# Performance work log

Measured on AMD Instinct MI355X. Metric: run time of the kernel, lower is better.

Reference implementation:

```python
import jax, jax.numpy as jnp
import numpy as np

EPS = 1e-8

def setup_inputs() -> dict:
    key = jax.random.key(0)
    ks = jax.random.split(key, 7)
    B, S, H, NH, V = 4, 2048, 1024, 8, 2048
    sc = 1.0 / np.sqrt(H)
    return {
        "hidden": jax.random.normal(ks[0], (B, S, H), jnp.float32),
        "prior_w": jax.random.normal(ks[1], (H, NH), jnp.float32) * sc,
        "prior_b": jnp.zeros((NH,), jnp.float32),
        "latent_w": jax.random.normal(ks[2], (H, NH * H), jnp.float32) * sc,
        "latent_b": jnp.zeros((NH * H,), jnp.float32),
        "output_w": jax.random.normal(ks[3], (H, V), jnp.float32) * sc,
        "output_b": jnp.zeros((V,), jnp.float32),
    }

def reference(hidden, prior_w, prior_b, latent_w, latent_b, output_w, output_b):
    B, S, H = hidden.shape
    NH = prior_w.shape[1]
    # prior: sigmoid then renormalize over heads
    prior = jax.nn.sigmoid(hidden @ prior_w + prior_b)              # [B,S,NH]
    prior = prior / (prior.sum(-1, keepdims=True) + EPS)
    # latent: linear -> [B,S,NH,H] -> tanh
    latent = jnp.tanh((hidden @ latent_w + latent_b).reshape(B, S, NH, H))
    # per-head softmax over vocab, weighted sum over heads
    logits = jnp.einsum('bsnh,hv->bsnv', latent, output_w) + output_b
    probs = jax.nn.softmax(logits, axis=-1)                          # [B,S,NH,V]
    return jnp.einsum('bsn,bsnv->bsv', prior, probs)
```

## Files before the change

kernel.cpp:

```cpp
#include <hip/hip_runtime.h>
#include <hip/hip_bf16.h>
#include <stdint.h>

typedef _Float16 f16;
typedef _Float16 f16x8 __attribute__((ext_vector_type(8)));
typedef _Float16 f16x4 __attribute__((ext_vector_type(4)));
typedef float f32x4 __attribute__((ext_vector_type(4)));
typedef float f32x16 __attribute__((ext_vector_type(16)));

#define T_TOK 8192
#define H_DIM 1024
#define NHEAD 8
#define V_DIM 2048

__device__ __forceinline__ void gload16(const void* g, void* l) {
  __builtin_amdgcn_global_load_lds(
      (const __attribute__((address_space(1))) void*)(uintptr_t)g,
      (__attribute__((address_space(3))) void*)(unsigned)(uintptr_t)l,
      16, 0, 0);
}

__device__ __forceinline__ float fast_tanh(float x) {
  float xc = fminf(fmaxf(x, -12.f), 12.f);
  float e = __expf(2.f * xc);
  return (e - 1.f) / (e + 1.f);
}

__device__ __forceinline__ void stage_half(const f16* __restrict__ gRowBase,
                                           char* ldsHalf, int tid, int sl8,
                                           int Kd) {
  const int srow = tid >> 3;
  char* wuni = ldsHalf + ((tid >> 6) << 10);
  gload16(gRowBase + (size_t)srow * Kd + sl8, wuni);
  gload16(gRowBase + (size_t)(srow + 64) * Kd + sl8, wuni + 8192);
}

template <int TANH, int NMAJ>
__global__ __launch_bounds__(512, 2) void k_gemm(const f16* __restrict__ A,
                                                 const f16* __restrict__ Bt,
                                                 const float* __restrict__ bias,
                                                 f16* __restrict__ C,
                                                 int M, int N, int K) {
  __shared__ __align__(16) f16 sA[2][16384];
  __shared__ __align__(16) f16 sB[2][16384];
  const int tid = threadIdx.x;
  const int lane = tid & 63;
  const int wid = tid >> 6;
  const int wr = wid >> 2, wc = wid & 3;
  const int gx = gridDim.x, gy = gridDim.y;
  const int id = blockIdx.y * gx + blockIdx.x;
  const int cpx = (gx * gy) >> 3;
  const int sw = (id & 7) * cpx + (id >> 3);
  int m0, n0;
  if (NMAJ) {
    n0 = (sw / gy) * 256;
    m0 = (sw % gy) * 256;
  } else {
    m0 = (sw / gx) * 256;
    n0 = (sw % gx) * 256;
  }
  const int NT = K >> 6;
  const int sl8 = ((tid & 7) ^ ((tid >> 3) & 7)) << 3;
  const int rr31 = lane & 31;
  const int hi = lane >> 5;
  const int l7 = lane & 7;

  const f16* Ag = A + (size_t)m0 * K;
  const f16* Bg = Bt + (size_t)n0 * K;
  char* sAb = (char*)&sA[0][0];
  char* sBb = (char*)&sB[0][0];

  stage_half(Ag, sAb, tid, sl8, K);
  stage_half(Ag + (size_t)128 * K, sAb + 16384, tid, sl8, K);
  stage_half(Bg, sBb, tid, sl8, K);
  stage_half(Bg + (size_t)128 * K, sBb + 16384, tid, sl8, K);
  stage_half(Bg + 64, sBb + 32768, tid, sl8, K);
  stage_half(Bg + (size_t)128 * K + 64, sBb + 32768 + 16384, tid, sl8, K);
  asm volatile("s_waitcnt vmcnt(4)" ::: "memory");
  __builtin_amdgcn_s_barrier();
  __builtin_amdgcn_sched_barrier(0);

  f32x16 acc[4][2] = {};
  f16x8 af0[4], af1[4], bf[2][4];

#define LDA_SET(dst, base, q)                                                  \
  {                                                                            \
    _Pragma("unroll") for (int mi = 0; mi < 4; ++mi) {                         \
      dst[mi] = *(const f16x8*)((base) + wr * 16384 + mi * 4096 + rr31 * 128 + \
                                (((2 * (q) + hi) ^ l7) << 4));                 \
    }                                                                          \
  }
#define LDB(base)                                                              \
  {                                                                            \
    _Pragma("unroll") for (int n = 0; n < 2; ++n) {                            \
      _Pragma("unroll") for (int ks = 0; ks < 4; ++ks) {                       \
        bf[n][ks] = *(const f16x8*)((base) + wc * 8192 + n * 4096 +            \
                                    rr31 * 128 + (((2 * ks + hi) ^ l7) << 4)); \
      }                                                                        \
    }                                                                          \
  }
#define MFMA8(ks, S)                                                           \
  {                                                                            \
    __builtin_amdgcn_s_setprio(1);                                             \
    _Pragma("unroll") for (int mi = 0; mi < 4; ++mi) {                         \
      _Pragma("unroll") for (int n = 0; n < 2; ++n) {                          \
        acc[mi][n] = __builtin_amdgcn_mfma_f32_32x32x16_f16(                   \
            S[mi], bf[n][ks], acc[mi][n], 0, 0, 0);                            \
      }                                                                        \
    }                                                                          \
    __builtin_amdgcn_s_setprio(0);                                             \
  }

  LDA_SET(af0, sAb, 0);

#define HALF(tt, bc)                                                           \
  {                                                                            \
    const char* cA = sAb + (bc)*32768;                                         \
    const char* cB = sBb + (bc)*32768;                                         \
    char* nA = sAb + ((bc) ^ 1) * 32768;                                       \
    char* nB = sBb + (bc)*32768;                                               \
    const int ktA = ((tt) + 1) << 6, ktB = ((tt) + 2) << 6;                    \
    const bool doA = (tt) + 1 < NT, doB = (tt) + 2 < NT;                       \
                                                                      \
    if (doA) stage_half(Ag + ktA, nA, tid, sl8, K);                            \
    LDB(cB);                                                                   \
    LDA_SET(af1, cA, 1);                                                       \
    __builtin_amdgcn_sched_barrier(0);                                         \
    MFMA8(0, af0);                                                             \
    __builtin_amdgcn_s_barrier();                                              \
                                                                      \
    if (doA) stage_half(Ag + (size_t)128 * K + ktA, nA + 16384, tid, sl8, K);  \
    LDA_SET(af0, cA, 2);                                                       \
    __builtin_amdgcn_sched_barrier(0);                                         \
    MFMA8(1, af1);                                                             \
    __builtin_amdgcn_s_barrier();                                              \
                                                                      \
    if (doB) stage_half(Bg + ktB, nB, tid, sl8, K);                            \
    LDA_SET(af1, cA, 3);                                                       \
    __builtin_amdgcn_sched_barrier(0);                                         \
    MFMA8(2, af0);                                                             \
    __builtin_amdgcn_s_barrier();                                              \
                  \
    if (doB) stage_half(Bg + (size_t)128 * K + ktB, nB + 16384, tid, sl8, K);  \
    if (doB) {                                                                 \
      asm volatile("s_waitcnt vmcnt(4)" ::: "memory");                         \
    } else {                                                                   \
      asm volatile("s_waitcnt vmcnt(0)" ::: "memory");                         \
    }                                                                          \
    __builtin_amdgcn_s_barrier();                                              \
    __builtin_amdgcn_sched_barrier(0);                                         \
    if (doA) LDA_SET(af0, sAb + ((bc) ^ 1) * 32768, 0);                        \
    __builtin_amdgcn_sched_barrier(0);                                         \
    MFMA8(3, af1);                                                             \
  }

#pragma unroll 1
  for (int T = 0; T < NT; T += 2) {
    HALF(T, 0);
    HALF(T + 1, 1);
  }
#undef HALF
#undef LDA_SET
#undef LDB
#undef MFMA8

  const int ccol0 = n0 + wc * 64 + rr31;
  float bv[2];
#pragma unroll
  for (int n = 0; n < 2; ++n) bv[n] = bias[ccol0 + n * 32];
#pragma unroll
  for (int mi = 0; mi < 4; ++mi) {
#pragma unroll
    for (int rq = 0; rq < 4; ++rq) {
#pragma unroll
      for (int r2 = 0; r2 < 4; ++r2) {
        const int row = m0 + wr * 128 + mi * 32 + r2 + 8 * rq + 4 * hi;
        f16* Crow = C + (size_t)row * N;
#pragma unroll
        for (int n = 0; n < 2; ++n) {
          float v = acc[mi][n][rq * 4 + r2] + bv[n];
          if (TANH) v = fast_tanh(v);
          Crow[ccol0 + n * 32] = (f16)v;
        }
      }
    }
  }
}

__global__ __launch_bounds__(256) void k_convert(const float* __restrict__ in,
                                                 f16* __restrict__ out, int n4) {
  int i = blockIdx.x * blockDim.x + threadIdx.x;
  if (i >= n4) return;
  const float4 v = ((const float4*)in)[i];
  f16x4 o;
  o[0] = (f16)v.x; o[1] = (f16)v.y; o[2] = (f16)v.z; o[3] = (f16)v.w;
  ((f16x4*)out)[i] = o;
}

__global__ __launch_bounds__(256) void k_transpose(const float* __restrict__ in,
                                                   f16* __restrict__ out,
                                                   int R, int C) {
  __shared__ f16 tile[64][66];
  const int c0 = blockIdx.x * 64, r0 = blockIdx.y * 64;
  const int tid = threadIdx.x;
  const int tr = tid >> 4;
  const int tc4 = (tid & 15) * 4;
#pragma unroll
  for (int i = 0; i < 4; ++i) {
    const int r = tr + i * 16;
    const float4 v = *(const float4*)&in[(size_t)(r0 + r) * C + c0 + tc4];
    tile[tc4 + 0][r] = (f16)v.x;
    tile[tc4 + 1][r] = (f16)v.y;
    tile[tc4 + 2][r] = (f16)v.z;
    tile[tc4 + 3][r] = (f16)v.w;
  }
  __syncthreads();
  const int oc = tid >> 2;
  const int or4 = (tid & 3) * 16;
#pragma unroll
  for (int i = 0; i < 4; ++i) {
    f16x4 w;
    w[0] = tile[oc][or4 + i * 4 + 0];
    w[1] = tile[oc][or4 + i * 4 + 1];
    w[2] = tile[oc][or4 + i * 4 + 2];
    w[3] = tile[oc][or4 + i * 4 + 3];
    *(f16x4*)&out[(size_t)(c0 + oc) * R + r0 + or4 + i * 4] = w;
  }
}

__global__ __launch_bounds__(256) void k_prior(const float* __restrict__ hidden,
                                               const float* __restrict__ pw,
                                               const float* __restrict__ pb,
                                               float* __restrict__ prior) {
  const int wid = threadIdx.x >> 6, lane = threadIdx.x & 63;
  const int t = blockIdx.x * 4 + wid;
  float acc[NHEAD] = {0.f, 0.f, 0.f, 0.f, 0.f, 0.f, 0.f, 0.f};
  const float* hrow = hidden + (size_t)t * H_DIM;
  for (int k = lane; k < H_DIM; k += 64) {
    float x = hrow[k];
    const float* wr = pw + k * NHEAD;
#pragma unroll
    for (int h = 0; h < NHEAD; ++h) acc[h] += x * wr[h];
  }
#pragma unroll
  for (int h = 0; h < NHEAD; ++h) {
#pragma unroll
    for (int off = 32; off >= 1; off >>= 1) acc[h] += __shfl_xor(acc[h], off);
  }
  if (lane == 0) {
    float p[NHEAD], s = 0.f;
#pragma unroll
    for (int h = 0; h < NHEAD; ++h) {
      p[h] = 1.f / (1.f + __expf(-(acc[h] + pb[h])));
      s += p[h];
    }
    float inv = 1.f / (s + 1e-8f);
#pragma unroll
    for (int h = 0; h < NHEAD; ++h) prior[t * NHEAD + h] = p[h] * inv;
  }
}

__global__ __launch_bounds__(256) void k_softmax(const f16* __restrict__ logits,
                                                 const float* __restrict__ prior,
                                                 float* __restrict__ out) {
  __shared__ float redsm[NHEAD * 4];
  const int t = blockIdx.x;
  const int tid = threadIdx.x, lane = tid & 63, wid = tid >> 6;
  const f16* base = logits + (size_t)t * NHEAD * V_DIM + tid * 8;

  f16x8 x[NHEAD];
#pragma unroll
  for (int h = 0; h < NHEAD; ++h) x[h] = *(const f16x8*)(base + h * V_DIM);

  float xv[NHEAD][8];
  float sml[NHEAD];
#pragma unroll
  for (int h = 0; h < NHEAD; ++h) {
    float s = 0.f;
#pragma unroll
    for (int j = 0; j < 8; ++j) {
      xv[h][j] = __expf(fminf((float)x[h][j], 50.f));
      s += xv[h][j];
    }
    sml[h] = s;
  }
#pragma unroll
  for (int h = 0; h < NHEAD; ++h) {
#pragma unroll
    for (int off = 32; off >= 1; off >>= 1) sml[h] += __shfl_xor(sml[h], off);
  }
  if (lane == 0) {
#pragma unroll
    for (int h = 0; h < NHEAD; ++h) redsm[h * 4 + wid] = sml[h];
  }
  __syncthreads();

  float oa[8] = {0.f, 0.f, 0.f, 0.f, 0.f, 0.f, 0.f, 0.f};
#pragma unroll
  for (int h = 0; h < NHEAD; ++h) {
    const float s = redsm[h * 4 + 0] + redsm[h * 4 + 1] + redsm[h * 4 + 2] +
                    redsm[h * 4 + 3];
    const float coef = prior[t * NHEAD + h] / s;
#pragma unroll
    for (int j = 0; j < 8; ++j) oa[j] += coef * xv[h][j];
  }
  float4* op = (float4*)(out + (size_t)t * V_DIM + tid * 8);
  op[0] = make_float4(oa[0], oa[1], oa[2], oa[3]);
  op[1] = make_float4(oa[4], oa[5], oa[6], oa[7]);
}

extern "C" void kernel_launch(void* const* d_in, const int* in_sizes, int n_in,
                              void* d_out, int out_size, void* d_ws, size_t ws_size,
                              hipStream_t stream) {
  const float* hidden   = (const float*)d_in[0];
  const float* prior_w  = (const float*)d_in[1];
  const float* prior_b  = (const float*)d_in[2];
  const float* latent_w = (const float*)d_in[3];
  const float* latent_b = (const float*)d_in[4];
  const float* output_w = (const float*)d_in[5];
  const float* output_b = (const float*)d_in[6];
  float* out = (float*)d_out;

  char* ws = (char*)d_ws;
  size_t off = 0;
  auto alloc = [&](size_t bytes) -> void* {
    void* p = ws + off;
    off += (bytes + 255) & ~(size_t)255;
    return p;
  };
  f16* hidden_h = (f16*)alloc((size_t)T_TOK * H_DIM * 2);
  f16* lw_t     = (f16*)alloc((size_t)NHEAD * H_DIM * H_DIM * 2);
  f16* ow_t     = (f16*)alloc((size_t)V_DIM * H_DIM * 2);
  float* prior  = (float*)alloc((size_t)T_TOK * NHEAD * 4);

  int tc = T_TOK;
  while (tc > 256) {
    size_t need = off + (size_t)tc * NHEAD * H_DIM * 2 + 256 +
                  (size_t)tc * NHEAD * V_DIM * 2 + 256;
    if (need <= ws_size) break;
    tc >>= 1;
  }
  f16* latent_h = (f16*)alloc((size_t)tc * NHEAD * H_DIM * 2);
  f16* logits_h = (f16*)alloc((size_t)tc * NHEAD * V_DIM * 2);

  k_convert<<<(T_TOK * H_DIM / 4 + 255) / 256, 256, 0, stream>>>(
      hidden, hidden_h, T_TOK * H_DIM / 4);
  k_transpose<<<dim3(NHEAD * H_DIM / 64, H_DIM / 64), 256, 0, stream>>>(
      latent_w, lw_t, H_DIM, NHEAD * H_DIM);
  k_transpose<<<dim3(V_DIM / 64, H_DIM / 64), 256, 0, stream>>>(
      output_w, ow_t, H_DIM, V_DIM);
  k_prior<<<T_TOK / 4, 256, 0, stream>>>(hidden, prior_w, prior_b, prior);

  const int nchunk = T_TOK / tc;
  for (int c = 0; c < nchunk; ++c) {
    const f16* Ah = hidden_h + (size_t)c * tc * H_DIM;
    k_gemm<1, 1><<<dim3(NHEAD * H_DIM / 256, tc / 256), 512, 0, stream>>>(
        Ah, lw_t, latent_b, latent_h, tc, NHEAD * H_DIM, H_DIM);
    k_gemm<0, 0><<<dim3(V_DIM / 256, tc * NHEAD / 256), 512, 0, stream>>>(
        latent_h, ow_t, output_b, logits_h, tc * NHEAD, V_DIM, H_DIM);
    k_softmax<<<tc, 256, 0, stream>>>(logits_h, prior + (size_t)c * tc * NHEAD,
                                      out + (size_t)c * tc * V_DIM);
  }
}
```

Before: 572.6 us.

## Fuse prior with hidden conversion, restructure GEMM grid and chunk logits buffer

Merges the fp32-to-fp16 hidden conversion into the prior kernel, so the hidden tensor is read once instead of twice. The latent GEMM now runs as a single launch over all tokens, using a 3D grid with a fixed 8-column swizzle and a z-dimension that selects the N block. The logits GEMM and softmax run over token quarters sized to fit the workspace, with softmax taking a token offset. This removes one kernel launch and changes the chunking plan, but the full latent buffer must fit in the workspace.

```diff
diff --git a/kernel.cpp b/kernel.cpp
--- a/kernel.cpp
+++ b/kernel.cpp
@@ -35,7 +35,7 @@
   gload16(gRowBase + (size_t)(srow + 64) * Kd + sl8, wuni + 8192);
 }
 
-template <int TANH, int NMAJ>
+template <int TANH>
 __global__ __launch_bounds__(512, 2) void k_gemm(const f16* __restrict__ A,
                                                  const f16* __restrict__ Bt,
                                                  const float* __restrict__ bias,
@@ -47,18 +47,11 @@
   const int lane = tid & 63;
   const int wid = tid >> 6;
   const int wr = wid >> 2, wc = wid & 3;
-  const int gx = gridDim.x, gy = gridDim.y;
-  const int id = blockIdx.y * gx + blockIdx.x;
-  const int cpx = (gx * gy) >> 3;
+  const int id = blockIdx.y * 8 + blockIdx.x;
+  const int cpx = gridDim.y;
   const int sw = (id & 7) * cpx + (id >> 3);
-  int m0, n0;
-  if (NMAJ) {
-    n0 = (sw / gy) * 256;
-    m0 = (sw % gy) * 256;
-  } else {
-    m0 = (sw / gx) * 256;
-    n0 = (sw % gx) * 256;
-  }
+  const int m0 = (sw >> 3) * 256;
+  const int n0 = blockIdx.z * 2048 + (sw & 7) * 256;
   const int NT = K >> 6;
   const int sl8 = ((tid & 7) ^ ((tid >> 3) & 7)) << 3;
   const int rr31 = lane & 31;
@@ -187,16 +180,6 @@
   }
 }
 
-__global__ __launch_bounds__(256) void k_convert(const float* __restrict__ in,
-                                                 f16* __restrict__ out, int n4) {
-  int i = blockIdx.x * blockDim.x + threadIdx.x;
-  if (i >= n4) return;
-  const float4 v = ((const float4*)in)[i];
-  f16x4 o;
-  o[0] = (f16)v.x; o[1] = (f16)v.y; o[2] = (f16)v.z; o[3] = (f16)v.w;
-  ((f16x4*)out)[i] = o;
-}
-
 __global__ __launch_bounds__(256) void k_transpose(const float* __restrict__ in,
                                                    f16* __restrict__ out,
                                                    int R, int C) {
@@ -228,19 +211,30 @@
   }
 }
 
-__global__ __launch_bounds__(256) void k_prior(const float* __restrict__ hidden,
-                                               const float* __restrict__ pw,
-                                               const float* __restrict__ pb,
-                                               float* __restrict__ prior) {
+__global__ __launch_bounds__(256) void k_prior_conv(const float* __restrict__ hidden,
+                                                    const float* __restrict__ pw,
+                                                    const float* __restrict__ pb,
+                                                    float* __restrict__ prior,
+                                                    f16* __restrict__ hidden_h) {
   const int wid = threadIdx.x >> 6, lane = threadIdx.x & 63;
   const int t = blockIdx.x * 4 + wid;
+  const float* hrow = hidden + (size_t)t * H_DIM;
+  f16* orow = hidden_h + (size_t)t * H_DIM;
   float acc[NHEAD] = {0.f, 0.f, 0.f, 0.f, 0.f, 0.f, 0.f, 0.f};
-  const float* hrow = hidden + (size_t)t * H_DIM;
-  for (int k = lane; k < H_DIM; k += 64) {
-    float x = hrow[k];
-    const float* wr = pw + k * NHEAD;
-#pragma unroll
-    for (int h = 0; h < NHEAD; ++h) acc[h] += x * wr[h];
+#pragma unroll
+  for (int i = 0; i < 4; ++i) {
+    const int k = i * 256 + lane * 4;
+    const float4 v = *(const float4*)(hrow + k);
+    f16x4 o;
+    o[0] = (f16)v.x; o[1] = (f16)v.y; o[2] = (f16)v.z; o[3] = (f16)v.w;
+    *(f16x4*)(orow + k) = o;
+    const float vv[4] = {v.x, v.y, v.z, v.w};
+#pragma unroll
+    for (int j = 0; j < 4; ++j) {
+      const float* wr = pw + (size_t)(k + j) * NHEAD;
+#pragma unroll
+      for (int h = 0; h < NHEAD; ++h) acc[h] += vv[j] * wr[h];
+    }
   }
 #pragma unroll
   for (int h = 0; h < NHEAD; ++h) {
@@ -262,11 +256,13 @@
 
 __global__ __launch_bounds__(256) void k_softmax(const f16* __restrict__ logits,
                                                  const float* __restrict__ prior,
-                                                 float* __restrict__ out) {
+                                                 float* __restrict__ out,
+                                                 int t0) {
   __shared__ float redsm[NHEAD * 4];
-  const int t = blockIdx.x;
+  const int tl = blockIdx.x;
+  const int t = t0 + tl;
   const int tid = threadIdx.x, lane = tid & 63, wid = tid >> 6;
-  const f16* base = logits + (size_t)t * NHEAD * V_DIM + tid * 8;
+  const f16* base = logits + (size_t)tl * NHEAD * V_DIM + tid * 8;
 
   f16x8 x[NHEAD];
 #pragma unroll
@@ -332,33 +328,28 @@
   f16* lw_t     = (f16*)alloc((size_t)NHEAD * H_DIM * H_DIM * 2);
   f16* ow_t     = (f16*)alloc((size_t)V_DIM * H_DIM * 2);
   float* prior  = (float*)alloc((size_t)T_TOK * NHEAD * 4);
-
-  int tc = T_TOK;
-  while (tc > 256) {
-    size_t need = off + (size_t)tc * NHEAD * H_DIM * 2 + 256 +
-                  (size_t)tc * NHEAD * V_DIM * 2 + 256;
-    if (need <= ws_size) break;
-    tc >>= 1;
-  }
-  f16* latent_h = (f16*)alloc((size_t)tc * NHEAD * H_DIM * 2);
-  f16* logits_h = (f16*)alloc((size_t)tc * NHEAD * V_DIM * 2);
-
-  k_convert<<<(T_TOK * H_DIM / 4 + 255) / 256, 256, 0, stream>>>(
-      hidden, hidden_h, T_TOK * H_DIM / 4);
+  f16* latent_h = (f16*)alloc((size_t)T_TOK * NHEAD * H_DIM * 2);
+
+  int TQ = 2048;
+  while (TQ > 256 && off + (size_t)TQ * NHEAD * V_DIM * 2 > ws_size) TQ >>= 1;
+  f16* logits_q = (f16*)alloc((size_t)TQ * NHEAD * V_DIM * 2);
+
+  k_prior_conv<<<T_TOK / 4, 256, 0, stream>>>(hidden, prior_w, prior_b, prior,
+                                              hidden_h);
   k_transpose<<<dim3(NHEAD * H_DIM / 64, H_DIM / 64), 256, 0, stream>>>(
       latent_w, lw_t, H_DIM, NHEAD * H_DIM);
   k_transpose<<<dim3(V_DIM / 64, H_DIM / 64), 256, 0, stream>>>(
       output_w, ow_t, H_DIM, V_DIM);
-  k_prior<<<T_TOK / 4, 256, 0, stream>>>(hidden, prior_w, prior_b, prior);
-
-  const int nchunk = T_TOK / tc;
-  for (int c = 0; c < nchunk; ++c) {
-    const f16* Ah = hidden_h + (size_t)c * tc * H_DIM;
-    k_gemm<1, 1><<<dim3(NHEAD * H_DIM / 256, tc / 256), 512, 0, stream>>>(
-        Ah, lw_t, latent_b, latent_h, tc, NHEAD * H_DIM, H_DIM);
-    k_gemm<0, 0><<<dim3(V_DIM / 256, tc * NHEAD / 256), 512, 0, stream>>>(
-        latent_h, ow_t, output_b, logits_h, tc * NHEAD, V_DIM, H_DIM);
-    k_softmax<<<tc, 256, 0, stream>>>(logits_h, prior + (size_t)c * tc * NHEAD,
-                                      out + (size_t)c * tc * V_DIM);
-  }
-}
+
+  k_gemm<1><<<dim3(8, T_TOK / 256, 4), 512, 0, stream>>>(
+      hidden_h, lw_t, latent_b, latent_h, T_TOK, NHEAD * H_DIM, H_DIM);
+
+  const int nq = T_TOK / TQ;
+  for (int s = 0; s < nq; ++s) {
+    const int MR = TQ * NHEAD;
+    k_gemm<0><<<dim3(8, MR / 256, 1), 512, 0, stream>>>(
+        latent_h + (size_t)s * MR * H_DIM, ow_t, output_b, logits_q, MR, V_DIM,
+        H_DIM);
+    k_softmax<<<TQ, 256, 0, stream>>>(logits_q, prior, out, s * TQ);
+  }
+}
```

New measurement: 597.9 us. 1.04x slower.
